# Optimization experiments

Hardware: AMD Instinct MI355X
Metric: run time of the kernel (lower is better)

The kernel has to match this reference:

```python
import jax, jax.numpy as jnp
import numpy as np

FP8_MAX = 448.0  # max finite value of float8_e4m3fn


def setup_inputs() -> dict:
    key = jax.random.key(0)
    k1, k2, k3 = jax.random.split(key, 3)
    B, S, D_IN, D_OUT = 2, 4096, 2048, 8192
    x = jax.random.normal(k1, (B, S, D_IN), dtype=jnp.float32)
    # Weight is stored pre-quantized in fp8 (per-tensor scale), layout (in, out)
    w_fp32 = jax.random.normal(k2, (D_IN, D_OUT), dtype=jnp.float32) * 0.02
    weight_scale = jnp.float32(jnp.max(jnp.abs(w_fp32)) / FP8_MAX)
    weight = jnp.clip(w_fp32 / weight_scale, -FP8_MAX, FP8_MAX).astype(jnp.float8_e4m3fn)
    input_scale = jnp.float32(0.05)  # static per-tensor activation scale
    bias = jax.random.normal(k3, (D_OUT,), dtype=jnp.float32)
    return {"x": x, "weight": weight, "weight_scale": weight_scale,
            "input_scale": input_scale, "bias": bias}


def reference(x, weight, weight_scale, input_scale, bias):
    # static_quantize_e4m3_per_tensor: q = cast_fp8(clip(x / s)), returns (q, s)
    q = jnp.clip(x / input_scale, -FP8_MAX, FP8_MAX).astype(jnp.float8_e4m3fn)
    q2d = q.reshape(-1, q.shape[-1]).astype(jnp.float32)  # [B*S, D_in]
    w = weight.astype(jnp.float32)                         # [D_in, D_out]
    # cublas_scaled_mm: (q @ w) * scale_a * scale_b, out in x.dtype
    out = jnp.matmul(q2d, w) * (input_scale * weight_scale)
    out = out.astype(x.dtype) + bias.astype(x.dtype)
    return out.reshape(x.shape[:-1] + (out.shape[-1],))
```

## Files before the change

### kernel.cpp

```cpp
#include <hip/hip_runtime.h>

typedef __attribute__((ext_vector_type(4))) float floatx4;

__device__ __forceinline__ unsigned int pack4_fp8(float f0, float f1, float f2, float f3) {
    int v = __builtin_amdgcn_cvt_pk_fp8_f32(f0, f1, 0, false);
    v = __builtin_amdgcn_cvt_pk_fp8_f32(f2, f3, v, true);
    return (unsigned int)v;
}

__global__ void detect_kernel(const unsigned int* __restrict__ W, int* __restrict__ flag) {
    __shared__ int ok[2];
    if (threadIdx.x == 0) { ok[0] = 1; ok[1] = 1; }
    __syncthreads();
    int f32ok = 1, bf16ok = 1;
#pragma unroll
    for (int i = 0; i < 16; ++i) {
        unsigned int w = W[threadIdx.x * 16 + i];
        if (w & 0x000FFFFFu) f32ok = 0;
        if (w & 0x000F000Fu) bf16ok = 0;
    }
    if (!f32ok)  atomicAnd(&ok[0], 0);
    if (!bf16ok) atomicAnd(&ok[1], 0);
    __syncthreads();
    if (threadIdx.x == 0) *flag = ok[0] ? 2 : (ok[1] ? 1 : 0);
}

__global__ void quant_kernel(const float* __restrict__ x,
                             unsigned int* __restrict__ q,
                             const float* __restrict__ iscale, int n8) {
    int i = blockIdx.x * blockDim.x + threadIdx.x;
    if (i >= n8) return;
    float s = iscale[0];
    const float4* xv = (const float4*)x;
    float4 a = xv[2 * i];
    float4 b = xv[2 * i + 1];
    float v[8] = {a.x, a.y, a.z, a.w, b.x, b.y, b.z, b.w};
#pragma unroll
    for (int j = 0; j < 8; ++j) {
        float t = v[j] / s;
        v[j] = fminf(fmaxf(t, -448.0f), 448.0f);
    }
    q[2 * i]     = pack4_fp8(v[0], v[1], v[2], v[3]);
    q[2 * i + 1] = pack4_fp8(v[4], v[5], v[6], v[7]);
}

template <int MODE>
__global__ void ingest_kernel(const unsigned char* __restrict__ W,
                              unsigned char* __restrict__ Wt,
                              const int* __restrict__ flag, int K, int N) {
    if (*flag != MODE) return;
    __shared__ __align__(16) unsigned char tile[64][68];
    const int k0 = blockIdx.y * 64;
    const int n0 = blockIdx.x * 64;
    const int t = threadIdx.x;
    const int kr = t >> 2;
    const int cg = (t & 3) * 16;
    const size_t eidx = (size_t)(k0 + kr) * N + (n0 + cg);

    unsigned int w4[4];
    if constexpr (MODE == 0) {
        uint4 v = *(const uint4*)(W + eidx);
        w4[0] = v.x; w4[1] = v.y; w4[2] = v.z; w4[3] = v.w;
    } else if constexpr (MODE == 1) {
        const uint4* p = (const uint4*)((const unsigned short*)W + eidx);
        uint4 A0 = p[0], A1 = p[1];
        unsigned int uw[8] = {A0.x, A0.y, A0.z, A0.w, A1.x, A1.y, A1.z, A1.w};
#pragma unroll
        for (int g = 0; g < 4; ++g) {
            float f0 = __uint_as_float((uw[2 * g] & 0xFFFFu) << 16);
            float f1 = __uint_as_float((uw[2 * g] >> 16) << 16);
            float f2 = __uint_as_float((uw[2 * g + 1] & 0xFFFFu) << 16);
            float f3 = __uint_as_float((uw[2 * g + 1] >> 16) << 16);
            w4[g] = pack4_fp8(f0, f1, f2, f3);
        }
    } else {
        const float4* p = (const float4*)((const float*)W + eidx);
#pragma unroll
        for (int g = 0; g < 4; ++g) {
            float4 f = p[g];
            w4[g] = pack4_fp8(f.x, f.y, f.z, f.w);
        }
    }
#pragma unroll
    for (int g = 0; g < 4; ++g)
        *(unsigned int*)&tile[kr][cg + 4 * g] = w4[g];
    __syncthreads();

    const int nr = t >> 2;
    const int kg = (t & 3) * 16;
    uint4 o;
    unsigned int w[4];
#pragma unroll
    for (int g = 0; g < 4; ++g) {
        unsigned int b0 = tile[kg + g * 4 + 0][nr];
        unsigned int b1 = tile[kg + g * 4 + 1][nr];
        unsigned int b2 = tile[kg + g * 4 + 2][nr];
        unsigned int b3 = tile[kg + g * 4 + 3][nr];
        w[g] = b0 | (b1 << 8) | (b2 << 16) | (b3 << 24);
    }
    o.x = w[0]; o.y = w[1]; o.z = w[2]; o.w = w[3];
    *(uint4*)(Wt + (size_t)(n0 + nr) * K + k0 + kg) = o;
}

__global__ __launch_bounds__(256) void gemm_fp8_kernel(
    const unsigned char* __restrict__ A,
    const unsigned char* __restrict__ Bt,
    float* __restrict__ C,
    const float* __restrict__ bias,
    const float* __restrict__ wscale,
    const float* __restrict__ iscale,
    int M, int N, int K) {
    constexpr int ROWB = 80;
    __shared__ __align__(16) unsigned char As[128 * ROWB];
    __shared__ __align__(16) unsigned char Bs[128 * ROWB];

    const int tid  = threadIdx.x;
    const int lane = tid & 63;
    const int wave = tid >> 6;
    const int wm = wave >> 1;
    const int wn = wave & 1;
    const int bm = blockIdx.y * 128;
    const int bn = blockIdx.x * 128;

    floatx4 acc[4][4] = {};

    const int c0 = tid, c1 = tid + 256;
    const int r0 = c0 >> 2, o0 = (c0 & 3) * 16;
    const int r1 = c1 >> 2, o1 = (c1 & 3) * 16;
    const unsigned char* pa0 = A  + (size_t)(bm + r0) * K + o0;
    const unsigned char* pa1 = A  + (size_t)(bm + r1) * K + o1;
    const unsigned char* pb0 = Bt + (size_t)(bn + r0) * K + o0;
    const unsigned char* pb1 = Bt + (size_t)(bn + r1) * K + o1;
    uint4* const sa0 = (uint4*)&As[r0 * ROWB + o0];
    uint4* const sa1 = (uint4*)&As[r1 * ROWB + o1];
    uint4* const sb0 = (uint4*)&Bs[r0 * ROWB + o0];
    uint4* const sb1 = (uint4*)&Bs[r1 * ROWB + o1];

    const int arow = wm * 64 + (lane & 15);
    const int brow = wn * 64 + (lane & 15);
    const int aq8  = (lane >> 4) * 8;

    for (int k0 = 0; k0 < K; k0 += 64) {
        uint4 va0 = *(const uint4*)pa0; pa0 += 64;
        uint4 va1 = *(const uint4*)pa1; pa1 += 64;
        uint4 vb0 = *(const uint4*)pb0; pb0 += 64;
        uint4 vb1 = *(const uint4*)pb1; pb1 += 64;
        __syncthreads();
        *sa0 = va0; *sa1 = va1;
        *sb0 = vb0; *sb1 = vb1;
        __syncthreads();

        long af[2][4], bf[2][4];
#pragma unroll
        for (int im = 0; im < 4; ++im) {
            af[0][im] = *(const long*)&As[(arow + im * 16) * ROWB + aq8];
            af[1][im] = *(const long*)&As[(arow + im * 16) * ROWB + aq8 + 32];
            bf[0][im] = *(const long*)&Bs[(brow + im * 16) * ROWB + aq8];
            bf[1][im] = *(const long*)&Bs[(brow + im * 16) * ROWB + aq8 + 32];
        }

#pragma unroll
        for (int ks = 0; ks < 2; ++ks)
#pragma unroll
            for (int im = 0; im < 4; ++im)
#pragma unroll
                for (int in = 0; in < 4; ++in)
                    acc[im][in] = __builtin_amdgcn_mfma_f32_16x16x32_fp8_fp8(
                        af[ks][im], bf[ks][in], acc[im][in], 0, 0, 0);
    }

    const float scale = iscale[0] * wscale[0];
    const int row0 = bm + wm * 64 + ((lane >> 4) << 2);
    const int col0 = bn + wn * 64 + (lane & 15);
#pragma unroll
    for (int in = 0; in < 4; ++in) {
        const int col = col0 + in * 16;
        const float bv = bias[col];
#pragma unroll
        for (int im = 0; im < 4; ++im) {
            const int row = row0 + im * 16;
            float* cp = C + (size_t)row * N + col;
#pragma unroll
            for (int r = 0; r < 4; ++r)
                cp[(size_t)r * N] = acc[im][in][r] * scale + bv;
        }
    }
}

extern "C" void kernel_launch(void* const* d_in, const int* in_sizes, int n_in,
                              void* d_out, int out_size, void* d_ws, size_t ws_size,
                              hipStream_t stream) {
    const float* x          = (const float*)d_in[0];
    const unsigned char* w  = (const unsigned char*)d_in[1];
    const float* wscale     = (const float*)d_in[2];
    const float* iscale     = (const float*)d_in[3];
    const float* bias       = (const float*)d_in[4];
    float* out              = (float*)d_out;

    const int D_OUT = in_sizes[4];
    const int D_IN  = in_sizes[1] / D_OUT;
    const int M     = in_sizes[0] / D_IN;

    int* flag         = (int*)d_ws;
    unsigned char* q  = (unsigned char*)d_ws + 256;
    unsigned char* wt = q + (size_t)M * D_IN;

    detect_kernel<<<1, 256, 0, stream>>>((const unsigned int*)w, flag);
    const int n8 = (M * D_IN) / 8;
    quant_kernel<<<(n8 + 255) / 256, 256, 0, stream>>>(x, (unsigned int*)q, iscale, n8);
    dim3 tg(D_OUT / 64, D_IN / 64);
    ingest_kernel<0><<<tg, 256, 0, stream>>>(w, wt, flag, D_IN, D_OUT);
    ingest_kernel<1><<<tg, 256, 0, stream>>>(w, wt, flag, D_IN, D_OUT);
    ingest_kernel<2><<<tg, 256, 0, stream>>>(w, wt, flag, D_IN, D_OUT);
    gemm_fp8_kernel<<<dim3(D_OUT / 128, M / 128), 256, 0, stream>>>(
        q, wt, out, bias, wscale, iscale, M, D_OUT, D_IN);
}
```

Measured before the change: 600.7 us.

## Switch GEMM to scaled 16x16x128 MFMA with LDS double buffering

Replaces the fp8 GEMM inner loop with the MI355X scaled MFMA 16x16x128 f8f6f4 instruction using unit scales, so each instruction covers four times the K depth. Tiles are fetched with direct global-to-LDS loads into a double buffer in a fragment-friendly layout, with a grid swizzle for L2 locality and launch bounds of 2 blocks per CU. The three mode-specific ingest launches are merged into one kernel that branches on the flag. This targets MFMA issue count, register staging of loads and launch overhead, at the cost of 64KB LDS per block, which may limit occupancy.

```diff
diff --git a/kernel.cpp b/kernel.cpp
--- a/kernel.cpp
+++ b/kernel.cpp
@@ -1,11 +1,18 @@
 #include <hip/hip_runtime.h>
 
 typedef __attribute__((ext_vector_type(4))) float floatx4;
+typedef __attribute__((ext_vector_type(8))) int   intx8;
 
 __device__ __forceinline__ unsigned int pack4_fp8(float f0, float f1, float f2, float f3) {
     int v = __builtin_amdgcn_cvt_pk_fp8_f32(f0, f1, 0, false);
     v = __builtin_amdgcn_cvt_pk_fp8_f32(f2, f3, v, true);
     return (unsigned int)v;
+}
+
+__device__ __forceinline__ void gload16(const unsigned char* g, unsigned char* l) {
+    __builtin_amdgcn_global_load_lds(
+        (const __attribute__((address_space(1))) unsigned int*)g,
+        (__attribute__((address_space(3))) unsigned int*)l, 16, 0, 0);
 }
 
 __global__ void detect_kernel(const unsigned int* __restrict__ W, int* __restrict__ flag) {
@@ -45,11 +52,10 @@
 }
 
 template <int MODE>
-__global__ void ingest_kernel(const unsigned char* __restrict__ W,
-                              unsigned char* __restrict__ Wt,
-                              const int* __restrict__ flag, int K, int N) {
-    if (*flag != MODE) return;
-    __shared__ __align__(16) unsigned char tile[64][68];
+__device__ __forceinline__ void ingest_body(const unsigned char* __restrict__ W,
+                                            unsigned char* __restrict__ Wt,
+                                            int K, int N,
+                                            unsigned char (*tile)[68]) {
     const int k0 = blockIdx.y * 64;
     const int n0 = blockIdx.x * 64;
     const int t = threadIdx.x;
@@ -102,7 +108,17 @@
     *(uint4*)(Wt + (size_t)(n0 + nr) * K + k0 + kg) = o;
 }
 
-__global__ __launch_bounds__(256) void gemm_fp8_kernel(
+__global__ void ingest_kernel(const unsigned char* __restrict__ W,
+                              unsigned char* __restrict__ Wt,
+                              const int* __restrict__ flag, int K, int N) {
+    __shared__ __align__(16) unsigned char tile[64][68];
+    const int mode = *flag;
+    if (mode == 0)      ingest_body<0>(W, Wt, K, N, tile);
+    else if (mode == 1) ingest_body<1>(W, Wt, K, N, tile);
+    else                ingest_body<2>(W, Wt, K, N, tile);
+}
+
+__global__ __launch_bounds__(256, 2) void gemm_mxfp8_kernel(
     const unsigned char* __restrict__ A,
     const unsigned char* __restrict__ Bt,
     float* __restrict__ C,
@@ -110,68 +126,95 @@
     const float* __restrict__ wscale,
     const float* __restrict__ iscale,
     int M, int N, int K) {
-    constexpr int ROWB = 80;
-    __shared__ __align__(16) unsigned char As[128 * ROWB];
-    __shared__ __align__(16) unsigned char Bs[128 * ROWB];
+    __shared__ __align__(16) unsigned char As[2][16384];
+    __shared__ __align__(16) unsigned char Bs[2][16384];
 
     const int tid  = threadIdx.x;
     const int lane = tid & 63;
-    const int wave = tid >> 6;
-    const int wm = wave >> 1;
-    const int wn = wave & 1;
-    const int bm = blockIdx.y * 128;
-    const int bn = blockIdx.x * 128;
+    const int wv   = tid >> 6;
+    const int wm   = wv >> 1;
+    const int wn   = wv & 1;
+    const int r16  = lane & 15;
+    const int cq   = lane >> 4;
+
+    const int nbx  = gridDim.x;
+    const int nwg  = nbx * gridDim.y;
+    const int orig = blockIdx.y * nbx + blockIdx.x;
+    const int cpx  = nwg >> 3;
+    const int swz  = (orig & 7) * cpx + (orig >> 3);
+    const int bm   = (swz / nbx) * 128;
+    const int bn   = (swz % nbx) * 128;
+
+    const unsigned char* ga[4];
+    const unsigned char* gb[4];
+    int lo[4];
+#pragma unroll
+    for (int j = 0; j < 4; ++j) {
+        const int u   = wv * 4 + j;
+        const int rb  = u >> 1;
+        const int rg  = u & 1;
+        const int row = rb * 16 + r16;
+        const int col = cq * 32 + rg * 16;
+        ga[j] = A  + (size_t)(bm + row) * K + col;
+        gb[j] = Bt + (size_t)(bn + row) * K + col;
+        lo[j] = rb * 2048 + rg * 1024;
+    }
 
     floatx4 acc[4][4] = {};
 
-    const int c0 = tid, c1 = tid + 256;
-    const int r0 = c0 >> 2, o0 = (c0 & 3) * 16;
-    const int r1 = c1 >> 2, o1 = (c1 & 3) * 16;
-    const unsigned char* pa0 = A  + (size_t)(bm + r0) * K + o0;
-    const unsigned char* pa1 = A  + (size_t)(bm + r1) * K + o1;
-    const unsigned char* pb0 = Bt + (size_t)(bn + r0) * K + o0;
-    const unsigned char* pb1 = Bt + (size_t)(bn + r1) * K + o1;
-    uint4* const sa0 = (uint4*)&As[r0 * ROWB + o0];
-    uint4* const sa1 = (uint4*)&As[r1 * ROWB + o1];
-    uint4* const sb0 = (uint4*)&Bs[r0 * ROWB + o0];
-    uint4* const sb1 = (uint4*)&Bs[r1 * ROWB + o1];
-
-    const int arow = wm * 64 + (lane & 15);
-    const int brow = wn * 64 + (lane & 15);
-    const int aq8  = (lane >> 4) * 8;
-
-    for (int k0 = 0; k0 < K; k0 += 64) {
-        uint4 va0 = *(const uint4*)pa0; pa0 += 64;
-        uint4 va1 = *(const uint4*)pa1; pa1 += 64;
-        uint4 vb0 = *(const uint4*)pb0; pb0 += 64;
-        uint4 vb1 = *(const uint4*)pb1; pb1 += 64;
+#pragma unroll
+    for (int j = 0; j < 4; ++j) {
+        gload16(ga[j], &As[0][lo[j]]);
+        gload16(gb[j], &Bs[0][lo[j]]);
+        ga[j] += 128; gb[j] += 128;
+    }
+    __syncthreads();
+
+    const unsigned char* pa0 = &As[0][wm * 4 * 2048 + lane * 16];
+    const unsigned char* pb0 = &Bs[0][wn * 4 * 2048 + lane * 16];
+
+    union U8 { intx8 v; uint4 q[2]; };
+    const int NT = K >> 7;
+    int cur = 0;
+    for (int kt = 0; kt < NT; ++kt) {
+        if (kt + 1 < NT) {
+#pragma unroll
+            for (int j = 0; j < 4; ++j) {
+                gload16(ga[j], &As[cur ^ 1][lo[j]]);
+                gload16(gb[j], &Bs[cur ^ 1][lo[j]]);
+                ga[j] += 128; gb[j] += 128;
+            }
+        }
+        intx8 af[4], bf[4];
+#pragma unroll
+        for (int i = 0; i < 4; ++i) {
+            U8 ua, ub;
+            const unsigned char* qa = pa0 + cur * 16384 + i * 2048;
+            const unsigned char* qb = pb0 + cur * 16384 + i * 2048;
+            ua.q[0] = *(const uint4*)qa;
+            ua.q[1] = *(const uint4*)(qa + 1024);
+            ub.q[0] = *(const uint4*)qb;
+            ub.q[1] = *(const uint4*)(qb + 1024);
+            af[i] = ua.v;
+            bf[i] = ub.v;
+        }
+#pragma unroll
+        for (int im = 0; im < 4; ++im)
+#pragma unroll
+            for (int in = 0; in < 4; ++in)
+                acc[im][in] = __builtin_amdgcn_mfma_scale_f32_16x16x128_f8f6f4(
+                    af[im], bf[in], acc[im][in],
+                    0, 0,
+                    0, 0x7F7F7F7F,
+                    0, 0x7F7F7F7F);
         __syncthreads();
-        *sa0 = va0; *sa1 = va1;
-        *sb0 = vb0; *sb1 = vb1;
-        __syncthreads();
-
-        long af[2][4], bf[2][4];
-#pragma unroll
-        for (int im = 0; im < 4; ++im) {
-            af[0][im] = *(const long*)&As[(arow + im * 16) * ROWB + aq8];
-            af[1][im] = *(const long*)&As[(arow + im * 16) * ROWB + aq8 + 32];
-            bf[0][im] = *(const long*)&Bs[(brow + im * 16) * ROWB + aq8];
-            bf[1][im] = *(const long*)&Bs[(brow + im * 16) * ROWB + aq8 + 32];
-        }
-
-#pragma unroll
-        for (int ks = 0; ks < 2; ++ks)
-#pragma unroll
-            for (int im = 0; im < 4; ++im)
-#pragma unroll
-                for (int in = 0; in < 4; ++in)
-                    acc[im][in] = __builtin_amdgcn_mfma_f32_16x16x32_fp8_fp8(
-                        af[ks][im], bf[ks][in], acc[im][in], 0, 0, 0);
-    }
+        cur ^= 1;
+    }
+    (void)M;
 
     const float scale = iscale[0] * wscale[0];
-    const int row0 = bm + wm * 64 + ((lane >> 4) << 2);
-    const int col0 = bn + wn * 64 + (lane & 15);
+    const int row0 = bm + wm * 64 + (cq << 2);
+    const int col0 = bn + wn * 64 + r16;
 #pragma unroll
     for (int in = 0; in < 4; ++in) {
         const int col = col0 + in * 16;
@@ -209,9 +252,7 @@
     const int n8 = (M * D_IN) / 8;
     quant_kernel<<<(n8 + 255) / 256, 256, 0, stream>>>(x, (unsigned int*)q, iscale, n8);
     dim3 tg(D_OUT / 64, D_IN / 64);
-    ingest_kernel<0><<<tg, 256, 0, stream>>>(w, wt, flag, D_IN, D_OUT);
-    ingest_kernel<1><<<tg, 256, 0, stream>>>(w, wt, flag, D_IN, D_OUT);
-    ingest_kernel<2><<<tg, 256, 0, stream>>>(w, wt, flag, D_IN, D_OUT);
-    gemm_fp8_kernel<<<dim3(D_OUT / 128, M / 128), 256, 0, stream>>>(
+    ingest_kernel<<<tg, 256, 0, stream>>>(w, wt, flag, D_IN, D_OUT);
+    gemm_mxfp8_kernel<<<dim3(D_OUT / 128, M / 128), 256, 0, stream>>>(
         q, wt, out, bias, wscale, iscale, M, D_OUT, D_IN);
 }
```

Measured after the change: 601.8 us. About the same (+0.2%).
